# Kernel tuning notes

Measured on AMD Instinct MI355X. Metric: run time of the kernel, lower is better.

Reference implementation:

```python
import jax, jax.numpy as jnp
import numpy as np

FILLER = 10.1  # filler_value from __init__
B, C, L, KEEP = 128, 16, 16384, 12288


def setup_inputs() -> dict:
    key = jax.random.key(0)
    k1, k2, k3, k4 = jax.random.split(key, 4)
    x1 = jax.random.normal(k1, (B, C, 4096), dtype=jnp.float32)
    x2 = jax.random.normal(k2, (B, C, 4096), dtype=jnp.float32)
    x3 = jax.random.normal(k3, (B, C, L), dtype=jnp.float32)
    # Scatter exactly (L - KEEP) filler entries at random positions in every row,
    # so per-row compaction yields a uniform length KEEP (required by np.stack
    # in the original module).
    u = jax.random.uniform(k4, (B, C, L))
    ranks = jnp.argsort(jnp.argsort(u, axis=-1), axis=-1)  # random permutation ranks
    fill_mask = ranks < (L - KEEP)
    x3 = jnp.where(fill_mask, jnp.float32(FILLER), x3)
    return {"x1": x1, "x2": x2, "x3": x3, "keep_len": KEEP}


def reference(x1, x2, x3, keep_len):
    # Per-row stream compaction: drop entries equal to FILLER, keep original
    # order of survivors, output fixed length keep_len.
    is_filler = x3 == jnp.float32(FILLER)          # [B, C, L] bool
    # Stable argsort moves non-filler (False=0) to the front, order-preserving.
    order = jnp.argsort(is_filler, axis=-1, stable=True)  # [B, C, L]
    compacted = jnp.take_along_axis(x3, order, axis=-1)    # [B, C, L]
    return compacted[..., :keep_len]                        # [B, C, keep_len]
```

## Files before the change

kernel.cpp:

```cpp
#include <hip/hip_runtime.h>


#define FILLER_VAL 10.1f
constexpr int L_LEN    = 16384;
constexpr int KEEP_LEN = 12288;
constexpr int BLOCK    = 256;
constexpr int NW       = BLOCK / 64;
constexpr int CHUNK    = BLOCK * 4;
constexpr int NC       = L_LEN / CHUNK;
constexpr int NSEG     = NC * NW;

__global__ __launch_bounds__(BLOCK) void count_kernel(
    const float* __restrict__ x3, int* __restrict__ bases)
{
    const int row = blockIdx.x;
    const float* __restrict__ in = x3 + (size_t)row * L_LEN;

    const int tid  = threadIdx.x;
    const int lane = tid & 63;
    const int wid  = tid >> 6;

    __shared__ int cnt[NSEG];

    #pragma unroll
    for (int c = 0; c < NC; ++c) {
        float4 v = *reinterpret_cast<const float4*>(in + c * CHUNK + tid * 4);
        unsigned long long m0 = __ballot(v.x != FILLER_VAL);
        unsigned long long m1 = __ballot(v.y != FILLER_VAL);
        unsigned long long m2 = __ballot(v.z != FILLER_VAL);
        unsigned long long m3 = __ballot(v.w != FILLER_VAL);
        if (lane == 0)
            cnt[c * NW + wid] = __popcll(m0) + __popcll(m1)
                              + __popcll(m2) + __popcll(m3);
    }
    __syncthreads();

    if (tid < 64) {
        int own = cnt[tid];
        int x = own;
        #pragma unroll
        for (int d = 1; d < 64; d <<= 1) {
            int y = __shfl_up(x, d);
            if (lane >= d) x += y;
        }
        bases[row * NSEG + tid] = x - own;
    }
}

__global__ __launch_bounds__(BLOCK) void scatter_kernel(
    const float* __restrict__ x3, const int* __restrict__ bases,
    float* __restrict__ out)
{
    const int bid = blockIdx.x;
    const int row = bid >> 2;
    const int q   = bid & 3;

    const float* __restrict__ in = x3 + (size_t)row * L_LEN;
    float* __restrict__ o = out + (size_t)row * KEEP_LEN;
    const int* __restrict__ rb = bases + row * NSEG;

    const int tid  = threadIdx.x;
    const int lane = tid & 63;
    const int wid  = tid >> 6;
    const unsigned long long lt = (1ULL << lane) - 1ULL;

    #pragma unroll
    for (int i = 0; i < NC / 4; ++i) {
        const int c = q * (NC / 4) + i;
        float4 v = *reinterpret_cast<const float4*>(in + c * CHUNK + tid * 4);

        unsigned long long m0 = __ballot(v.x != FILLER_VAL);
        unsigned long long m1 = __ballot(v.y != FILLER_VAL);
        unsigned long long m2 = __ballot(v.z != FILLER_VAL);
        unsigned long long m3 = __ballot(v.w != FILLER_VAL);

        const int before = __popcll(m0 & lt) + __popcll(m1 & lt)
                         + __popcll(m2 & lt) + __popcll(m3 & lt);

        int pos = rb[c * NW + wid] + before;

        if (v.x != FILLER_VAL) { if (pos < KEEP_LEN) o[pos] = v.x; ++pos; }
        if (v.y != FILLER_VAL) { if (pos < KEEP_LEN) o[pos] = v.y; ++pos; }
        if (v.z != FILLER_VAL) { if (pos < KEEP_LEN) o[pos] = v.z; ++pos; }
        if (v.w != FILLER_VAL) { if (pos < KEEP_LEN) o[pos] = v.w; ++pos; }
    }
}

extern "C" void kernel_launch(void* const* d_in, const int* in_sizes, int n_in,
                              void* d_out, int out_size, void* d_ws, size_t ws_size,
                              hipStream_t stream)
{
    const float* x3 = (const float*)d_in[2];
    float* out = (float*)d_out;
    int* bases = (int*)d_ws;

    const int rows = in_sizes[2] / L_LEN;

    count_kernel<<<rows, BLOCK, 0, stream>>>(x3, bases);
    scatter_kernel<<<rows * 4, BLOCK, 0, stream>>>(x3, bases, out);
}
```

Measured before the change: 273.4 us.

## Split counting into quarter blocks and stage compacted output in LDS for coalesced writes

The count pass now runs four blocks per row, each writing segment counts, and a separate 64-thread kernel does the per-row prefix scan. This spreads the count work across more blocks. The scatter pass compacts each quarter into a shared-memory buffer and then writes it out contiguously, replacing scattered per-thread global stores with coalesced ones. The cost is a third kernel launch plus an extra workspace round trip for the counts.

After: 270.8 us. About the same (-1.0%).

```diff
diff --git a/kernel.cpp b/kernel.cpp
--- a/kernel.cpp
+++ b/kernel.cpp
@@ -5,85 +5,97 @@
 constexpr int L_LEN    = 16384;
 constexpr int KEEP_LEN = 12288;
 constexpr int BLOCK    = 256;
-constexpr int NW       = BLOCK / 64;
-constexpr int CHUNK    = BLOCK * 4;
-constexpr int NC       = L_LEN / CHUNK;
-constexpr int NSEG     = NC * NW;
+constexpr int QELEM    = 4096;
+constexpr int QCH      = 4;
+constexpr int NSEG     = 64;
 
-__global__ __launch_bounds__(BLOCK) void count_kernel(
-    const float* __restrict__ x3, int* __restrict__ bases)
+__global__ __launch_bounds__(BLOCK) void count_segs(
+    const float* __restrict__ x3, int* __restrict__ cnt)
 {
-    const int row = blockIdx.x;
-    const float* __restrict__ in = x3 + (size_t)row * L_LEN;
+    const int bid = blockIdx.x;
+    const int row = bid >> 2;
+    const int q   = bid & 3;
+    const float* __restrict__ in = x3 + (size_t)row * L_LEN + q * QELEM;
 
     const int tid  = threadIdx.x;
     const int lane = tid & 63;
     const int wid  = tid >> 6;
 
-    __shared__ int cnt[NSEG];
-
     #pragma unroll
-    for (int c = 0; c < NC; ++c) {
-        float4 v = *reinterpret_cast<const float4*>(in + c * CHUNK + tid * 4);
+    for (int c = 0; c < QCH; ++c) {
+        float4 v = *reinterpret_cast<const float4*>(in + c * (BLOCK * 4) + tid * 4);
         unsigned long long m0 = __ballot(v.x != FILLER_VAL);
         unsigned long long m1 = __ballot(v.y != FILLER_VAL);
         unsigned long long m2 = __ballot(v.z != FILLER_VAL);
         unsigned long long m3 = __ballot(v.w != FILLER_VAL);
         if (lane == 0)
-            cnt[c * NW + wid] = __popcll(m0) + __popcll(m1)
-                              + __popcll(m2) + __popcll(m3);
-    }
-    __syncthreads();
-
-    if (tid < 64) {
-        int own = cnt[tid];
-        int x = own;
-        #pragma unroll
-        for (int d = 1; d < 64; d <<= 1) {
-            int y = __shfl_up(x, d);
-            if (lane >= d) x += y;
-        }
-        bases[row * NSEG + tid] = x - own;
+            cnt[row * NSEG + q * 16 + c * 4 + wid] =
+                __popcll(m0) + __popcll(m1) + __popcll(m2) + __popcll(m3);
     }
 }
 
-__global__ __launch_bounds__(BLOCK) void scatter_kernel(
-    const float* __restrict__ x3, const int* __restrict__ bases,
+__global__ __launch_bounds__(64) void prefix_rows(
+    const int* __restrict__ cnt, int* __restrict__ base)
+{
+    const int row  = blockIdx.x;
+    const int lane = threadIdx.x;
+
+    const int own = cnt[row * NSEG + lane];
+    int x = own;
+    #pragma unroll
+    for (int d = 1; d < 64; d <<= 1) {
+        int y = __shfl_up(x, d);
+        if (lane >= d) x += y;
+    }
+    base[row * NSEG + lane] = x - own;
+}
+
+__global__ __launch_bounds__(BLOCK) void emit_quarters(
+    const float* __restrict__ x3, const int* __restrict__ base,
     float* __restrict__ out)
 {
     const int bid = blockIdx.x;
     const int row = bid >> 2;
     const int q   = bid & 3;
 
-    const float* __restrict__ in = x3 + (size_t)row * L_LEN;
+    const float* __restrict__ in = x3 + (size_t)row * L_LEN + q * QELEM;
     float* __restrict__ o = out + (size_t)row * KEEP_LEN;
-    const int* __restrict__ rb = bases + row * NSEG;
+    const int* __restrict__ rb = base + row * NSEG;
 
     const int tid  = threadIdx.x;
     const int lane = tid & 63;
     const int wid  = tid >> 6;
     const unsigned long long lt = (1ULL << lane) - 1ULL;
 
+    __shared__ float stage[QELEM];
+
+    const int blockbase = rb[q * 16];
+
     #pragma unroll
-    for (int i = 0; i < NC / 4; ++i) {
-        const int c = q * (NC / 4) + i;
-        float4 v = *reinterpret_cast<const float4*>(in + c * CHUNK + tid * 4);
-
+    for (int c = 0; c < QCH; ++c) {
+        float4 v = *reinterpret_cast<const float4*>(in + c * (BLOCK * 4) + tid * 4);
         unsigned long long m0 = __ballot(v.x != FILLER_VAL);
         unsigned long long m1 = __ballot(v.y != FILLER_VAL);
         unsigned long long m2 = __ballot(v.z != FILLER_VAL);
         unsigned long long m3 = __ballot(v.w != FILLER_VAL);
-
         const int before = __popcll(m0 & lt) + __popcll(m1 & lt)
                          + __popcll(m2 & lt) + __popcll(m3 & lt);
 
-        int pos = rb[c * NW + wid] + before;
+        int pos = rb[q * 16 + c * 4 + wid] - blockbase + before;
 
-        if (v.x != FILLER_VAL) { if (pos < KEEP_LEN) o[pos] = v.x; ++pos; }
-        if (v.y != FILLER_VAL) { if (pos < KEEP_LEN) o[pos] = v.y; ++pos; }
-        if (v.z != FILLER_VAL) { if (pos < KEEP_LEN) o[pos] = v.z; ++pos; }
-        if (v.w != FILLER_VAL) { if (pos < KEEP_LEN) o[pos] = v.w; ++pos; }
+        if (v.x != FILLER_VAL) { if (pos >= 0 && pos < QELEM) stage[pos] = v.x; ++pos; }
+        if (v.y != FILLER_VAL) { if (pos >= 0 && pos < QELEM) stage[pos] = v.y; ++pos; }
+        if (v.z != FILLER_VAL) { if (pos >= 0 && pos < QELEM) stage[pos] = v.z; ++pos; }
+        if (v.w != FILLER_VAL) { if (pos >= 0 && pos < QELEM) stage[pos] = v.w; ++pos; }
     }
+    __syncthreads();
+
+    int cnt = ((q == 3) ? KEEP_LEN : rb[q * 16 + 16]) - blockbase;
+    if (cnt > QELEM) cnt = QELEM;
+    if (blockbase + cnt > KEEP_LEN) cnt = KEEP_LEN - blockbase;
+
+    for (int i = tid; i < cnt; i += BLOCK)
+        o[blockbase + i] = stage[i];
 }
 
 extern "C" void kernel_launch(void* const* d_in, const int* in_sizes, int n_in,
@@ -92,10 +104,13 @@
 {
     const float* x3 = (const float*)d_in[2];
     float* out = (float*)d_out;
-    int* bases = (int*)d_ws;
 
     const int rows = in_sizes[2] / L_LEN;
 
-    count_kernel<<<rows, BLOCK, 0, stream>>>(x3, bases);
-    scatter_kernel<<<rows * 4, BLOCK, 0, stream>>>(x3, bases, out);
+    int* cnt  = (int*)d_ws;
+    int* bas  = cnt + (size_t)rows * NSEG;
+
+    count_segs  <<<rows * 4, BLOCK, 0, stream>>>(x3, cnt);
+    prefix_rows <<<rows,     64,    0, stream>>>(cnt, bas);
+    emit_quarters<<<rows * 4, BLOCK, 0, stream>>>(x3, bas, out);
 }
```
